# Performance work log

Measured on AMD Instinct MI355X. Metric: run time of the kernel, lower is better.

Reference implementation:

```python
import jax, jax.numpy as jnp
import numpy as np

N = 50000
E = 800000
D = 128
DOUT = 128
KEEP_SCALE = 2.0  # 1 / (1 - drop_rate), drop_rate = 0.5


def setup_inputs() -> dict:
    key = jax.random.key(0)
    k1, k2, k3, k4, k5, k6 = jax.random.split(key, 6)
    X = jax.random.normal(k1, (N, D), dtype=jnp.float32)
    W = jax.random.normal(k2, (2 * D, DOUT), dtype=jnp.float32) * (1.0 / np.sqrt(2 * D))
    b = jax.random.normal(k3, (DOUT,), dtype=jnp.float32) * 0.01
    src = jax.random.randint(k4, (E,), 0, N, dtype=jnp.int32)
    dst = jax.random.randint(k5, (E,), 0, N, dtype=jnp.int32)
    drop_mask = jax.random.randint(k6, (N, DOUT), 0, 2, dtype=jnp.int32)
    return {"X": X, "W": W, "b": b, "src": src, "dst": dst, "drop_mask": drop_mask}


def reference(X, W, b, src, dst, drop_mask):
    # v2v mean aggregation: X_nbr[i] = mean_{(j->i) in E} X[j]
    nbr_sum = jax.ops.segment_sum(X[src], dst, num_segments=N)        # [N, D]
    deg = jax.ops.segment_sum(jnp.ones((E,), X.dtype), dst, num_segments=N)  # [N]
    X_nbr = nbr_sum / jnp.maximum(deg, 1.0)[:, None]
    # concat + linear + relu + dropout (deterministic mask, train-mode scaling)
    H = jnp.concatenate([X, X_nbr], axis=1)                           # [N, 2D]
    out = jax.nn.relu(H @ W + b)
    out = out * (drop_mask.astype(out.dtype) * KEEP_SCALE)
    return out
```

## Files before the change

### kernel.cpp

```cpp
#include <hip/hip_runtime.h>

#define NN 50000
#define ND 50048
#define NW 6256
#define NE 800000
#define CHUNKS 32
#define EPC 25000
#define CAP 56
#define NTILE 3125
#define CVT_UNITS 1600000
#define CVT_BLOCKS 1563

typedef __attribute__((ext_vector_type(8))) short short8;
typedef __attribute__((ext_vector_type(4))) float f32x4;
typedef __attribute__((ext_vector_type(2))) float f32x2;
typedef __attribute__((ext_vector_type(4))) unsigned int u32x4;
typedef __attribute__((ext_vector_type(2))) unsigned int u32x2;


__device__ __forceinline__ unsigned f2bf(float f) {
  unsigned u = __builtin_bit_cast(unsigned, f);
  return (u + 0x7fffu + ((u >> 16) & 1u)) >> 16;
}

#if defined(__has_builtin) && __has_builtin(__builtin_amdgcn_cvt_pk_fp8_f32) && \
    __has_builtin(__builtin_amdgcn_cvt_pk_f32_fp8)
#define FP8_HW 1
#else
#define FP8_HW 0
#endif

#if !FP8_HW
__device__ __forceinline__ unsigned f2fp8(float x) {
  unsigned u = __builtin_bit_cast(unsigned, x);
  unsigned s = (u >> 24) & 0x80u;
  float a = __builtin_bit_cast(float, u & 0x7fffffffu);
  if (a < 0.015625f) {
    unsigned q = (unsigned)(a * 512.0f + 0.5f);
    return s | (q == 8u ? 0x08u : q);
  }
  if (a >= 448.0f) return s | 0x7Eu;
  unsigned v = u & 0x7fffffffu;
  v = v + 0x0007FFFFu + ((v >> 20) & 1u);
  unsigned e = (v >> 23) - 120u;
  if (e >= 16u) return s | 0x7Eu;
  return s | (e << 3) | ((v >> 20) & 7u);
}
__device__ __forceinline__ float fp82f(unsigned b) {
  unsigned s = (b & 0x80u) << 24;
  unsigned e = (b >> 3) & 15u;
  unsigned m = b & 7u;
  unsigned mag = e ? ((e + 120u) << 23) | (m << 20)
                   : __builtin_bit_cast(unsigned, (float)m * 0.001953125f);
  return __builtin_bit_cast(float, s | mag);
}
#endif

__global__ __launch_bounds__(1024) void k_rankconv(const int* __restrict__ dst,
                                                   const float* __restrict__ W,
                                                   const float* __restrict__ X,
                                                   unsigned char* __restrict__ rank,
                                                   unsigned int* __restrict__ chunkcnt,
                                                   u32x4* __restrict__ Wfrag,
                                                   u32x2* __restrict__ Xbf2,
                                                   unsigned int* __restrict__ Xf8w) {
  int tid = threadIdx.x;
  int c = blockIdx.x;
  if (c >= CHUNKS) {
    int i = (c - CHUNKS) * 1024 + tid;
    if (i < CVT_UNITS) {
      f32x4 v = ((const f32x4*)X)[i];
      u32x2 o;
      o[0] = f2bf(v[0]) | (f2bf(v[1]) << 16);
      o[1] = f2bf(v[2]) | (f2bf(v[3]) << 16);
      Xbf2[i] = o;
      unsigned p8;
#if FP8_HW
      p8 = __builtin_amdgcn_cvt_pk_fp8_f32(v[0], v[1], 0, false);
      p8 = __builtin_amdgcn_cvt_pk_fp8_f32(v[2], v[3], p8, true);
#else
      p8 = f2fp8(v[0]) | (f2fp8(v[1]) << 8) | (f2fp8(v[2]) << 16) | (f2fp8(v[3]) << 24);
#endif
      Xf8w[i] = p8;
    } else if (i < CVT_UNITS + 32) {
      Xbf2[i] = (u32x2){0u, 0u};
      Xf8w[i] = 0u;
    }
    return;
  }
  __shared__ unsigned int pack[NW];
  if (tid < 128) {
    int s = c * 128 + tid;
    int lane = s & 63;
    int t = (s >> 6) & 7;
    int kb = s >> 9;
    int col = t * 16 + (lane & 15);
    int k0 = kb * 32 + (lane >> 4) * 8;
    u32x4 o;
#pragma unroll
    for (int p = 0; p < 4; ++p) {
      unsigned lo = f2bf(W[(k0 + 2 * p) * 128 + col]);
      unsigned hi = f2bf(W[(k0 + 2 * p + 1) * 128 + col]);
      o[p] = lo | (hi << 16);
    }
    Wfrag[s] = o;
  }
  for (int w = tid; w < NW; w += 1024) pack[w] = 0;
  __syncthreads();
  int ebase = c * EPC;
  for (int i = tid; i < EPC; i += 1024) {
    int e = ebase + i;
    int d = dst[e];
    unsigned sh = (unsigned)(d & 7) * 4u;
    unsigned old = atomicAdd(&pack[d >> 3], 1u << sh);
    rank[e] = (unsigned char)((old >> sh) & 15u);
  }
  __syncthreads();
  for (int w = tid; w < NW; w += 1024) chunkcnt[(size_t)c * NW + w] = pack[w];
}

__global__ __launch_bounds__(64) void k_base(const unsigned int* __restrict__ chunkcnt,
                                             unsigned char* __restrict__ chunkbase,
                                             unsigned int* __restrict__ deg) {
  int d = blockIdx.x * 64 + threadIdx.x;
  if (d >= NN) return;
  int w = d >> 3;
  unsigned sh = (unsigned)(d & 7) * 4u;
  unsigned cnts[CHUNKS];
#pragma unroll
  for (int c = 0; c < CHUNKS; ++c) cnts[c] = chunkcnt[(size_t)c * NW + w];
  unsigned run = 0;
#pragma unroll
  for (int c = 0; c < CHUNKS; ++c) {
    chunkbase[(size_t)c * ND + d] = (unsigned char)run;
    run += (cnts[c] >> sh) & 15u;
  }
  deg[d] = run;
}

__global__ __launch_bounds__(256) void k_place(const int* __restrict__ src,
                                               const int* __restrict__ dst,
                                               const unsigned char* __restrict__ rank,
                                               const unsigned char* __restrict__ chunkbase,
                                               unsigned short* __restrict__ slots) {
  int e = blockIdx.x * 256 + threadIdx.x;
  if (e >= NE) return;
  int c = e / EPC;
  int d = dst[e];
  int pos = (int)chunkbase[(size_t)c * ND + d] + (int)rank[e];
  if (pos < CAP) slots[d * CAP + pos] = (unsigned short)src[e];
}

__global__ __launch_bounds__(256) void k_aggregate(const u32x4* __restrict__ Xf8_4,
                                                   const unsigned int* __restrict__ deg,
                                                   const unsigned short* __restrict__ slots,
                                                   u32x4* __restrict__ Xnbr4) {
  int lane = threadIdx.x & 63;
  int node = blockIdx.x * 4 + (threadIdx.x >> 6);
  int g = lane >> 3;
  int i = lane & 7;
  int dg = (int)deg[node];
  int m = min(dg, CAP);
  const unsigned short* sl = slots + node * CAP;
  int s_pre = sl[min(lane, CAP - 1)];
  float acc[16];
#pragma unroll
  for (int k = 0; k < 16; ++k) acc[k] = 0.f;

#define LOADB(bb, dstv)                                   \
  {                                                       \
    int e_ = (bb) * 8 + g;                                \
    int s_ = __shfl(s_pre, min(e_, CAP - 1), 64);         \
    s_ = (e_ < m) ? s_ : NN;                              \
    dstv = Xf8_4[(size_t)s_ * 8 + i];                     \
  }
#if FP8_HW
#define ACC(v)                                                          \
  {                                                                     \
    _Pragma("unroll") for (int w_ = 0; w_ < 4; ++w_) {                  \
      f32x2 lo_ = __builtin_amdgcn_cvt_pk_f32_fp8((int)v[w_], false);   \
      f32x2 hi_ = __builtin_amdgcn_cvt_pk_f32_fp8((int)v[w_], true);    \
      acc[4 * w_ + 0] += lo_[0];                                        \
      acc[4 * w_ + 1] += lo_[1];                                        \
      acc[4 * w_ + 2] += hi_[0];                                        \
      acc[4 * w_ + 3] += hi_[1];                                        \
    }                                                                   \
  }
#else
#define ACC(v)                                                          \
  {                                                                     \
    _Pragma("unroll") for (int w_ = 0; w_ < 4; ++w_) {                  \
      unsigned b_ = v[w_];                                              \
      acc[4 * w_ + 0] += fp82f(b_ & 255u);                              \
      acc[4 * w_ + 1] += fp82f((b_ >> 8) & 255u);                       \
      acc[4 * w_ + 2] += fp82f((b_ >> 16) & 255u);                      \
      acc[4 * w_ + 3] += fp82f(b_ >> 24);                               \
    }                                                                   \
  }
#endif

  int nb = (m + 7) >> 3;
  if (nb > 0) {
    u32x4 cur;
    LOADB(0, cur);
    if (nb > 1) {
      u32x4 nxt;
      LOADB(1, nxt);
      for (int bb = 2; bb < nb; ++bb) {
        u32x4 n2;
        LOADB(bb, n2);
        ACC(cur);
        cur = nxt;
        nxt = n2;
      }
      ACC(cur);
      cur = nxt;
    }
    ACC(cur);
  }
#undef LOADB
#undef ACC

#pragma unroll
  for (int k = 0; k < 16; ++k) acc[k] += __shfl_xor(acc[k], 8, 64);
#pragma unroll
  for (int k = 0; k < 16; ++k) acc[k] += __shfl_xor(acc[k], 16, 64);
#pragma unroll
  for (int k = 0; k < 16; ++k) acc[k] += __shfl_xor(acc[k], 32, 64);

  if (lane < 8) {
    float inv = 1.0f / (float)max(dg, 1);
    u32x4 o0, o1;
#pragma unroll
    for (int p = 0; p < 4; ++p) {
      o0[p] = f2bf(acc[2 * p] * inv) | (f2bf(acc[2 * p + 1] * inv) << 16);
      o1[p] = f2bf(acc[8 + 2 * p] * inv) | (f2bf(acc[9 + 2 * p] * inv) << 16);
    }
    Xnbr4[(size_t)node * 16 + i * 2] = o0;
    Xnbr4[(size_t)node * 16 + i * 2 + 1] = o1;
  }
}

__global__ __launch_bounds__(512) void k_gemm(const unsigned short* __restrict__ Xbf,
                                              const unsigned short* __restrict__ Xnbr,
                                              const u32x4* __restrict__ Wfrag,
                                              const float* __restrict__ b,
                                              const int* __restrict__ mask,
                                              float* __restrict__ out) {
  int lane = threadIdx.x & 63;
  int wid = threadIdx.x >> 6;
  int tile = blockIdx.x * 8 + wid;
  if (tile >= NTILE) return;

  int row = tile * 16 + (lane & 15);
  const u32x4* a0 = (const u32x4*)(Xbf + (size_t)row * 128) + (lane >> 4);
  const u32x4* a1 = (const u32x4*)(Xnbr + (size_t)row * 128) + (lane >> 4);

  float bias[8];
#pragma unroll
  for (int t = 0; t < 8; ++t) bias[t] = b[t * 16 + (lane & 15)];

  f32x4 acc[8];
#pragma unroll
  for (int t = 0; t < 8; ++t) acc[t] = (f32x4){0.f, 0.f, 0.f, 0.f};

#pragma unroll
  for (int kb = 0; kb < 4; ++kb) {
    short8 a = __builtin_bit_cast(short8, a0[kb * 4]);
#pragma unroll
    for (int t = 0; t < 8; ++t) {
      short8 w = __builtin_bit_cast(short8, Wfrag[(kb * 8 + t) * 64 + lane]);
      acc[t] = __builtin_amdgcn_mfma_f32_16x16x32_bf16(a, w, acc[t], 0, 0, 0);
    }
  }
#pragma unroll
  for (int kb = 0; kb < 4; ++kb) {
    short8 a = __builtin_bit_cast(short8, a1[kb * 4]);
#pragma unroll
    for (int t = 0; t < 8; ++t) {
      short8 w = __builtin_bit_cast(short8, Wfrag[((kb + 4) * 8 + t) * 64 + lane]);
      acc[t] = __builtin_amdgcn_mfma_f32_16x16x32_bf16(a, w, acc[t], 0, 0, 0);
    }
  }

  int orow = tile * 16 + (lane >> 4) * 4;
  int ocol = lane & 15;
#pragma unroll
  for (int t = 0; t < 8; ++t) {
#pragma unroll
    for (int rg = 0; rg < 4; ++rg) {
      size_t idx = (size_t)(orow + rg) * 128 + t * 16 + ocol;
      float v = fmaxf(acc[t][rg] + bias[t], 0.f);
      int mk = mask[idx];
      out[idx] = v * (2.0f * (float)mk);
    }
  }
}

extern "C" void kernel_launch(void* const* d_in, const int* in_sizes, int n_in,
                              void* d_out, int out_size, void* d_ws, size_t ws_size,
                              hipStream_t stream) {
  (void)in_sizes; (void)n_in; (void)out_size; (void)ws_size;
  const float* X = (const float*)d_in[0];
  const float* W = (const float*)d_in[1];
  const float* b = (const float*)d_in[2];
  const int* src = (const int*)d_in[3];
  const int* dst = (const int*)d_in[4];
  const int* mask = (const int*)d_in[5];
  float* out = (float*)d_out;

  char* ws = (char*)d_ws;
  u32x4* Wfrag = (u32x4*)ws;
  unsigned int* deg = (unsigned int*)(ws + 65536);
  unsigned short* slots = (unsigned short*)(ws + 265728);
  unsigned int* Xf8w = (unsigned int*)(ws + 5865728);
  const u32x4* Xf8_4 = (const u32x4*)(ws + 5865728);
  u32x2* Xbf2 = (u32x2*)(ws + 12265984);
  const unsigned short* Xbf = (const unsigned short*)(ws + 12265984);
  u32x4* Xnbr4 = (u32x4*)(ws + 25066240);
  const unsigned short* Xnbr = (const unsigned short*)(ws + 25066240);
  unsigned char* rank = (unsigned char*)(ws + 25066240);
  unsigned int* chunkcnt = (unsigned int*)(ws + 25866240);
  unsigned char* chunkbase = (unsigned char*)(ws + 26667008);

  k_rankconv<<<CHUNKS + CVT_BLOCKS, 1024, 0, stream>>>(dst, W, X, rank, chunkcnt, Wfrag,
                                                       Xbf2, Xf8w);
  k_base<<<(NN + 63) / 64, 64, 0, stream>>>(chunkcnt, chunkbase, deg);
  k_place<<<(NE + 255) / 256, 256, 0, stream>>>(src, dst, rank, chunkbase, slots);
  k_aggregate<<<NN / 4, 256, 0, stream>>>(Xf8_4, deg, slots, Xnbr4);
  k_gemm<<<(NTILE + 7) / 8, 512, 0, stream>>>(Xbf, Xnbr, Wfrag, b, mask, out);
}
```

Measured before the change: 82.63 us.

## Replace 8-edge-parallel aggregation with per-lane feature-pair gather over edges

The aggregation kernel is rewritten so each of the 64 lanes owns two fp8 features and loops over all neighbor edges, doing 2-byte loads per lane. Previously 8 edges were handled in parallel with 16-byte loads, followed by a three-level cross-lane shuffle reduction. The new form removes that shuffle reduction and the 16-register accumulators, and every lane writes its own output word. The cost is narrow 2-byte loads and a serial edge loop per wave. The conversion kernel's zero-padding branch is also merged into the main path.

```diff
diff --git a/kernel.cpp b/kernel.cpp
--- a/kernel.cpp
+++ b/kernel.cpp
@@ -68,8 +68,9 @@
   int c = blockIdx.x;
   if (c >= CHUNKS) {
     int i = (c - CHUNKS) * 1024 + tid;
-    if (i < CVT_UNITS) {
-      f32x4 v = ((const f32x4*)X)[i];
+    if (i < CVT_UNITS + 32) {
+      f32x4 v = (f32x4){0.f, 0.f, 0.f, 0.f};
+      if (i < CVT_UNITS) v = ((const f32x4*)X)[i];
       u32x2 o;
       o[0] = f2bf(v[0]) | (f2bf(v[1]) << 16);
       o[1] = f2bf(v[2]) | (f2bf(v[3]) << 16);
@@ -82,9 +83,6 @@
       p8 = f2fp8(v[0]) | (f2fp8(v[1]) << 8) | (f2fp8(v[2]) << 16) | (f2fp8(v[3]) << 24);
 #endif
       Xf8w[i] = p8;
-    } else if (i < CVT_UNITS + 32) {
-      Xbf2[i] = (u32x2){0u, 0u};
-      Xf8w[i] = 0u;
     }
     return;
   }
@@ -151,94 +149,42 @@
   if (pos < CAP) slots[d * CAP + pos] = (unsigned short)src[e];
 }
 
-__global__ __launch_bounds__(256) void k_aggregate(const u32x4* __restrict__ Xf8_4,
-                                                   const unsigned int* __restrict__ deg,
-                                                   const unsigned short* __restrict__ slots,
-                                                   u32x4* __restrict__ Xnbr4) {
+__global__ __launch_bounds__(256) void k_gather(const unsigned short* __restrict__ Xf8u,
+                                                const unsigned int* __restrict__ deg,
+                                                const unsigned short* __restrict__ slots,
+                                                unsigned int* __restrict__ Xnbr32) {
   int lane = threadIdx.x & 63;
   int node = blockIdx.x * 4 + (threadIdx.x >> 6);
-  int g = lane >> 3;
-  int i = lane & 7;
   int dg = (int)deg[node];
   int m = min(dg, CAP);
   const unsigned short* sl = slots + node * CAP;
   int s_pre = sl[min(lane, CAP - 1)];
-  float acc[16];
-#pragma unroll
-  for (int k = 0; k < 16; ++k) acc[k] = 0.f;
-
-#define LOADB(bb, dstv)                                   \
-  {                                                       \
-    int e_ = (bb) * 8 + g;                                \
-    int s_ = __shfl(s_pre, min(e_, CAP - 1), 64);         \
-    s_ = (e_ < m) ? s_ : NN;                              \
-    dstv = Xf8_4[(size_t)s_ * 8 + i];                     \
-  }
+  float a0 = 0.f, a1 = 0.f;
+
+  for (int e0 = 0; e0 < m; e0 += 8) {
+    int cnt = m - e0;
+    unsigned short v[8];
+#pragma unroll
+    for (int j = 0; j < 8; ++j) {
+      int s_ = __shfl(s_pre, e0 + j, 64);
+      s_ = (j < cnt) ? s_ : NN;
+      v[j] = Xf8u[(size_t)s_ * 64 + lane];
+    }
+#pragma unroll
+    for (int j = 0; j < 8; ++j) {
 #if FP8_HW
-#define ACC(v)                                                          \
-  {                                                                     \
-    _Pragma("unroll") for (int w_ = 0; w_ < 4; ++w_) {                  \
-      f32x2 lo_ = __builtin_amdgcn_cvt_pk_f32_fp8((int)v[w_], false);   \
-      f32x2 hi_ = __builtin_amdgcn_cvt_pk_f32_fp8((int)v[w_], true);    \
-      acc[4 * w_ + 0] += lo_[0];                                        \
-      acc[4 * w_ + 1] += lo_[1];                                        \
-      acc[4 * w_ + 2] += hi_[0];                                        \
-      acc[4 * w_ + 3] += hi_[1];                                        \
-    }                                                                   \
-  }
+      f32x2 p = __builtin_amdgcn_cvt_pk_f32_fp8((int)(unsigned)v[j], false);
+      a0 += p[0];
+      a1 += p[1];
 #else
-#define ACC(v)                                                          \
-  {                                                                     \
-    _Pragma("unroll") for (int w_ = 0; w_ < 4; ++w_) {                  \
-      unsigned b_ = v[w_];                                              \
-      acc[4 * w_ + 0] += fp82f(b_ & 255u);                              \
-      acc[4 * w_ + 1] += fp82f((b_ >> 8) & 255u);                       \
-      acc[4 * w_ + 2] += fp82f((b_ >> 16) & 255u);                      \
-      acc[4 * w_ + 3] += fp82f(b_ >> 24);                               \
-    }                                                                   \
-  }
-#endif
-
-  int nb = (m + 7) >> 3;
-  if (nb > 0) {
-    u32x4 cur;
-    LOADB(0, cur);
-    if (nb > 1) {
-      u32x4 nxt;
-      LOADB(1, nxt);
-      for (int bb = 2; bb < nb; ++bb) {
-        u32x4 n2;
-        LOADB(bb, n2);
-        ACC(cur);
-        cur = nxt;
-        nxt = n2;
-      }
-      ACC(cur);
-      cur = nxt;
-    }
-    ACC(cur);
-  }
-#undef LOADB
-#undef ACC
-
-#pragma unroll
-  for (int k = 0; k < 16; ++k) acc[k] += __shfl_xor(acc[k], 8, 64);
-#pragma unroll
-  for (int k = 0; k < 16; ++k) acc[k] += __shfl_xor(acc[k], 16, 64);
-#pragma unroll
-  for (int k = 0; k < 16; ++k) acc[k] += __shfl_xor(acc[k], 32, 64);
-
-  if (lane < 8) {
-    float inv = 1.0f / (float)max(dg, 1);
-    u32x4 o0, o1;
-#pragma unroll
-    for (int p = 0; p < 4; ++p) {
-      o0[p] = f2bf(acc[2 * p] * inv) | (f2bf(acc[2 * p + 1] * inv) << 16);
-      o1[p] = f2bf(acc[8 + 2 * p] * inv) | (f2bf(acc[9 + 2 * p] * inv) << 16);
-    }
-    Xnbr4[(size_t)node * 16 + i * 2] = o0;
-    Xnbr4[(size_t)node * 16 + i * 2 + 1] = o1;
-  }
+      unsigned b_ = v[j];
+      a0 += fp82f(b_ & 255u);
+      a1 += fp82f((b_ >> 8) & 255u);
+#endif
+    }
+  }
+  float inv = 1.0f / (float)max(dg, 1);
+  Xnbr32[(size_t)node * 64 + lane] = f2bf(a0 * inv) | (f2bf(a1 * inv) << 16);
 }
 
 __global__ __launch_bounds__(512) void k_gemm(const unsigned short* __restrict__ Xbf,
@@ -314,10 +260,10 @@
   unsigned int* deg = (unsigned int*)(ws + 65536);
   unsigned short* slots = (unsigned short*)(ws + 265728);
   unsigned int* Xf8w = (unsigned int*)(ws + 5865728);
-  const u32x4* Xf8_4 = (const u32x4*)(ws + 5865728);
+  const unsigned short* Xf8u = (const unsigned short*)(ws + 5865728);
   u32x2* Xbf2 = (u32x2*)(ws + 12265984);
   const unsigned short* Xbf = (const unsigned short*)(ws + 12265984);
-  u32x4* Xnbr4 = (u32x4*)(ws + 25066240);
+  unsigned int* Xnbr32 = (unsigned int*)(ws + 25066240);
   const unsigned short* Xnbr = (const unsigned short*)(ws + 25066240);
   unsigned char* rank = (unsigned char*)(ws + 25066240);
   unsigned int* chunkcnt = (unsigned int*)(ws + 25866240);
@@ -327,6 +273,6 @@
                                                        Xbf2, Xf8w);
   k_base<<<(NN + 63) / 64, 64, 0, stream>>>(chunkcnt, chunkbase, deg);
   k_place<<<(NE + 255) / 256, 256, 0, stream>>>(src, dst, rank, chunkbase, slots);
-  k_aggregate<<<NN / 4, 256, 0, stream>>>(Xf8_4, deg, slots, Xnbr4);
+  k_gather<<<NN / 4, 256, 0, stream>>>(Xf8u, deg, slots, Xnbr32);
   k_gemm<<<(NTILE + 7) / 8, 512, 0, stream>>>(Xbf, Xnbr, Wfrag, b, mask, out);
 }
```

Result: faster. 74.69 us (-9.6%).
